# Optimization experiments

Hardware: AMD Instinct MI355X
Metric: run time of the kernel (lower is better)

Reference implementation:

```python
import jax, jax.numpy as jnp
import numpy as np

B, S, D, H = 2, 2048, 1024, 16  # batch, pad_size, depth, num_heads
HD = D // H


def setup_inputs() -> dict:
    key = jax.random.key(0)
    ks = jax.random.split(key, 20)
    g = lambda k, shape, fan: jax.random.normal(k, shape, jnp.float32) * np.sqrt(2.0 / fan)
    return {
        "x": jax.random.normal(ks[0], (B, S, D), jnp.float32),
        "W_in": g(ks[1], (D, D), 2 * D), "b_in": g(ks[2], (D,), D),
        "Wq": g(ks[3], (D, D), 2 * D), "bq": g(ks[4], (D,), D),
        "Wk": g(ks[5], (D, D), 2 * D), "bk": g(ks[6], (D,), D),
        "Wv": g(ks[7], (D, D), 2 * D), "bv": g(ks[8], (D,), D),
        "Wo": g(ks[9], (D, D), 2 * D), "bo": g(ks[10], (D,), D),
        "W1": g(ks[11], (D, D), 2 * D), "b1": g(ks[12], (D,), D),
        "W2": g(ks[13], (D, D), 2 * D), "b2": g(ks[14], (D,), D),
        # residual gate scalars (random_id_att / random_id_ff); zero-init in the
        # original, set nonzero here so the whole graph contributes.
        "s_att": jax.random.normal(ks[15], (), jnp.float32),
        "s_ff": jax.random.normal(ks[16], (), jnp.float32),
    }


def reference(x, W_in, b_in, Wq, bq, Wk, bk, Wv, bv, Wo, bo, W1, b1, W2, b2, s_att, s_ff):
    # input projection
    h = x @ W_in + b_in                                   # [B,S,D]
    # QKV projections, split heads -> [B,H,S,HD]
    def heads(t):
        return t.reshape(B, S, H, HD).transpose(0, 2, 1, 3)
    q = heads(h @ Wq + bq)
    k = heads(h @ Wk + bk)
    v = heads(h @ Wv + bv)
    # attention: sigmoid(logits) * tanh(logits) instead of softmax
    logits = jnp.einsum("bhqd,bhkd->bhqk", q, k) / jnp.sqrt(jnp.float32(D))
    attn = jax.nn.sigmoid(logits) * jnp.tanh(logits)      # [B,H,S,S]
    ctx = jnp.einsum("bhqk,bhkd->bhqd", attn, v)
    ctx = ctx.transpose(0, 2, 1, 3).reshape(B, S, D)
    attention = ctx @ Wo + bo
    # gated residual 1
    latent = h + s_att * attention
    # FFN (depth -> depth -> depth), leaky_relu alpha=0.2 (tf default);
    # dropout treated as identity (inference)
    ff = jax.nn.leaky_relu(latent @ W1 + b1, negative_slope=0.2) @ W2 + b2
    out = latent + s_ff * ff
    return out
```

## Files before the change

kernel.cpp:

```cpp
#include <hip/hip_runtime.h>
#include <cstdint>
#include <cstddef>


#define B_ 2
#define S_ 2048
#define D_ 1024
#define H_ 16
#define M_ 4096

typedef __attribute__((ext_vector_type(4))) float  f32x4;
typedef __attribute__((ext_vector_type(8))) __bf16 bf16x8;
typedef __attribute__((ext_vector_type(4))) __bf16 bf16x4;

__device__ __forceinline__ void async16(const void* g, void* l) {
    __builtin_amdgcn_global_load_lds(
        (__attribute__((address_space(1))) void*)(g),
        (__attribute__((address_space(3))) void*)(l), 16, 0, 0);
}

__device__ __forceinline__ float actf(float s) {
    float t = fminf(s * -0.045084223f, 21.6f);
    float u = __builtin_amdgcn_exp2f(t);
    return (1.f - u) * __builtin_amdgcn_rcpf(1.f + u * u);
}

template <int BM, int EPI>
__global__ __launch_bounds__(256) void gemm_k(
    const __bf16* __restrict__ A, const __bf16* __restrict__ Bt,
    const float* __restrict__ bias, const __bf16* __restrict__ aux,
    const float* __restrict__ scal, void* __restrict__ out, int Ntot)
{
    constexpr int K = D_;
    constexpr int MF = BM / 32;
    __shared__ __align__(16) __bf16 As[2][BM][64];
    __shared__ __align__(16) __bf16 Bs[2][128][64];

    const int tid = threadIdx.x, wid = tid >> 6, lane = tid & 63;
    const int wr = wid >> 1, wc = wid & 1;
    const int m0 = blockIdx.x * BM, n0 = blockIdx.y * 128;
    const int frow = lane & 15;
    const int kb = (lane >> 4) * 16;
    char* cAs = (char*)As; char* cBs = (char*)Bs;

    f32x4 acc[MF][4] = {};

    auto stage = [&](int buf, int k0) {
        char* lA = cAs + buf * (BM * 128);
        char* lB = cBs + buf * (128 * 128);
#pragma unroll
        for (int i = 0; i < MF; ++i) {
            const int o = tid * 16 + i * 4096;
            const int row = o >> 7;
            const int cb = (o & 127) ^ ((row & 7) << 4);
            async16(A + (size_t)(m0 + row) * K + k0 + (cb >> 1), lA + o);
        }
#pragma unroll
        for (int i = 0; i < 4; ++i) {
            const int o = tid * 16 + i * 4096;
            const int row = o >> 7;
            const int cb = (o & 127) ^ ((row & 7) << 4);
            async16(Bt + (size_t)(n0 + row) * K + k0 + (cb >> 1), lB + o);
        }
    };

    stage(0, 0);
    __syncthreads();
    int cur = 0;

    for (int k0 = 0; k0 < K; k0 += 64) {
        if (k0 + 64 < K) stage(cur ^ 1, k0 + 64);
        char* lA = cAs + cur * (BM * 128);
        char* lB = cBs + cur * (128 * 128);
#pragma unroll
        for (int kk = 0; kk < 2; ++kk) {
            bf16x8 af[MF], bfr[4];
#pragma unroll
            for (int m = 0; m < MF; ++m) {
                const int r = wr * (BM / 2) + m * 16 + frow;
                af[m] = *(const bf16x8*)(lA + ((r * 128 + kk * 64 + kb) ^ ((r & 7) << 4)));
            }
#pragma unroll
            for (int n = 0; n < 4; ++n) {
                const int r = wc * 64 + n * 16 + frow;
                bfr[n] = *(const bf16x8*)(lB + ((r * 128 + kk * 64 + kb) ^ ((r & 7) << 4)));
            }
#pragma unroll
            for (int m = 0; m < MF; ++m)
#pragma unroll
                for (int n = 0; n < 4; ++n)
                    acc[m][n] = __builtin_amdgcn_mfma_f32_16x16x32_bf16(
                        af[m], bfr[n], acc[m][n], 0, 0, 0);
        }
        __syncthreads();
        cur ^= 1;
    }

    const float sv = (EPI >= 2) ? *scal : 0.f;
#pragma unroll
    for (int m = 0; m < MF; ++m) {
#pragma unroll
        for (int n = 0; n < 4; ++n) {
#pragma unroll
            for (int r = 0; r < 4; ++r) {
                const int row = m0 + wr * (BM / 2) + m * 16 + (lane >> 4) * 4 + r;
                const int col = n0 + wc * 64 + n * 16 + frow;
                const size_t idx = (size_t)row * Ntot + col;
                float v = acc[m][n][r] + bias[col];
                if constexpr (EPI == 0) {
                    ((__bf16*)out)[idx] = (__bf16)v;
                } else if constexpr (EPI == 1) {
                    v = v > 0.f ? v : 0.2f * v;
                    ((__bf16*)out)[idx] = (__bf16)v;
                } else if constexpr (EPI == 2) {
                    ((__bf16*)out)[idx] = (__bf16)((float)aux[idx] + sv * v);
                } else {
                    ((float*)out)[idx] = (float)aux[idx] + sv * v;
                }
            }
        }
    }
}

__global__ __launch_bounds__(256, 4) void attn_k(
    const __bf16* __restrict__ Q, const __bf16* __restrict__ Kmat,
    const __bf16* __restrict__ VT, __bf16* __restrict__ CTX, int ld)
{
    __shared__ __align__(16) __bf16 Ks[2][64][64];
    __shared__ __align__(16) __bf16 Vs[2][64][64];
    __shared__ __align__(16) __bf16 Ps[64][64];

    const int tid = threadIdx.x, wid = tid >> 6, lane = tid & 63;
    const int qt = blockIdx.x, h = blockIdx.y, b = blockIdx.z;
    const int q0 = qt * 64;
    const int frow = lane & 15, g = lane >> 4;
    const int kg8 = g * 8, kb = g * 16;
    const int qrow = wid * 16 + frow;

    const __bf16* qbase = Q    + (size_t)(b * S_ + q0) * ld + h * 64;
    const __bf16* kbase = Kmat + (size_t)b * S_ * ld + h * 64;
    const __bf16* vbase = VT   + (size_t)(b * H_ + h) * 64 * S_;

    bf16x8 qf[2];
#pragma unroll
    for (int kk = 0; kk < 2; ++kk)
        qf[kk] = *(const bf16x8*)(qbase + (size_t)qrow * ld + kk * 32 + kg8);

    f32x4 octx[4] = {};
    char* cKs = (char*)Ks; char* cVs = (char*)Vs; char* lPs = (char*)Ps;

    auto stageKV = [&](int buf, int kt) {
#pragma unroll
        for (int i = 0; i < 2; ++i) {
            const int o = tid * 16 + i * 4096;
            const int row = o >> 7;
            const int cb = (o & 127) ^ ((row & 7) << 4);
            async16(kbase + (size_t)(kt + row) * ld + (cb >> 1),
                    cKs + buf * 8192 + o);
            async16(vbase + (size_t)row * S_ + kt + (cb >> 1),
                    cVs + buf * 8192 + o);
        }
    };

    stageKV(0, 0);
    __syncthreads();
    int cur = 0;

    for (int kt = 0; kt < S_; kt += 64) {
        if (kt + 64 < S_) stageKV(cur ^ 1, kt + 64);
        char* lKs = cKs + cur * 8192;
        char* lVs = cVs + cur * 8192;

        f32x4 scc[4] = {};
#pragma unroll
        for (int kk = 0; kk < 2; ++kk) {
            bf16x8 kf[4];
#pragma unroll
            for (int n = 0; n < 4; ++n) {
                const int r = n * 16 + frow;
                kf[n] = *(const bf16x8*)(lKs + ((r * 128 + kk * 64 + kb) ^ ((r & 7) << 4)));
            }
#pragma unroll
            for (int n = 0; n < 4; ++n)
                scc[n] = __builtin_amdgcn_mfma_f32_16x16x32_bf16(
                    kf[n], qf[kk], scc[n], 0, 0, 0);
        }

#pragma unroll
        for (int n = 0; n < 4; ++n) {
            bf16x4 pw;
#pragma unroll
            for (int r = 0; r < 4; ++r) pw[r] = (__bf16)actf(scc[n][r]);
            *(bf16x4*)(lPs + ((qrow * 128 + n * 32 + g * 8) ^ ((qrow & 7) << 4))) = pw;
        }

#pragma unroll
        for (int ks = 0; ks < 2; ++ks) {
            bf16x8 pf = *(const bf16x8*)(lPs +
                ((qrow * 128 + ks * 64 + kb) ^ ((qrow & 7) << 4)));
            bf16x8 vf[4];
#pragma unroll
            for (int nd = 0; nd < 4; ++nd) {
                const int rd = nd * 16 + frow;
                vf[nd] = *(const bf16x8*)(lVs + ((rd * 128 + ks * 64 + kb) ^ ((rd & 7) << 4)));
            }
#pragma unroll
            for (int nd = 0; nd < 4; ++nd)
                octx[nd] = __builtin_amdgcn_mfma_f32_16x16x32_bf16(
                    pf, vf[nd], octx[nd], 0, 0, 0);
        }
        __syncthreads();
        cur ^= 1;
    }

#pragma unroll
    for (int nd = 0; nd < 4; ++nd)
#pragma unroll
        for (int r = 0; r < 4; ++r) {
            const int row = q0 + wid * 16 + g * 4 + r;
            const int col = h * 64 + nd * 16 + frow;
            CTX[(size_t)(b * S_ + row) * D_ + col] = (__bf16)octx[nd][r];
        }
}

struct WPack { const float* w[7]; };

__global__ __launch_bounds__(256) void conv_transpose_w(WPack p, __bf16* out) {
    __shared__ float t[32][33];
    const float* W = p.w[blockIdx.z];
    __bf16* o = out + (size_t)blockIdx.z * D_ * D_;
    const int c0 = blockIdx.x * 32, r0 = blockIdx.y * 32;
    const int tx = threadIdx.x, ty = threadIdx.y;
#pragma unroll
    for (int i = 0; i < 4; ++i)
        t[ty + i * 8][tx] = W[(size_t)(r0 + ty + i * 8) * D_ + c0 + tx];
    __syncthreads();
#pragma unroll
    for (int i = 0; i < 4; ++i)
        o[(size_t)(c0 + ty + i * 8) * D_ + r0 + tx] = (__bf16)t[tx][ty + i * 8];
}

__global__ __launch_bounds__(256) void conv_bf16(
    const float* __restrict__ in, __bf16* __restrict__ out, int n4)
{
    const int i = blockIdx.x * blockDim.x + threadIdx.x;
    if (i < n4) {
        f32x4 v = ((const f32x4*)in)[i];
        bf16x4 o;
        o[0] = (__bf16)v[0]; o[1] = (__bf16)v[1];
        o[2] = (__bf16)v[2]; o[3] = (__bf16)v[3];
        ((bf16x4*)out)[i] = o;
    }
}

__global__ __launch_bounds__(256) void bcat_k(
    const float* __restrict__ bq, const float* __restrict__ bk,
    const float* __restrict__ bv, float* __restrict__ o)
{
    const int i = blockIdx.x * 256 + threadIdx.x;
    o[i] = i < 1024 ? bq[i] : (i < 2048 ? bk[i - 1024] : bv[i - 2048]);
}

__global__ __launch_bounds__(256) void transpose_v(
    const __bf16* __restrict__ V, __bf16* __restrict__ VT, int ld)
{
    __shared__ __bf16 t[32][33];
    const int s0 = blockIdx.x * 32, c0 = blockIdx.y * 32, b = blockIdx.z;
    const int tx = threadIdx.x, ty = threadIdx.y;
#pragma unroll
    for (int i = 0; i < 4; ++i)
        t[ty + i * 8][tx] = V[(size_t)(b * S_ + s0 + ty + i * 8) * ld + c0 + tx];
    __syncthreads();
#pragma unroll
    for (int i = 0; i < 4; ++i)
        VT[(size_t)(b * D_ + c0 + ty + i * 8) * S_ + s0 + tx] = t[tx][ty + i * 8];
}

extern "C" void kernel_launch(void* const* d_in, const int* in_sizes, int n_in,
                              void* d_out, int out_size, void* d_ws, size_t ws_size,
                              hipStream_t stream) {
    const float* x    = (const float*)d_in[0];
    const float* W_in = (const float*)d_in[1];
    const float* b_in = (const float*)d_in[2];
    const float* Wq   = (const float*)d_in[3];
    const float* bq   = (const float*)d_in[4];
    const float* Wk   = (const float*)d_in[5];
    const float* bk   = (const float*)d_in[6];
    const float* Wv   = (const float*)d_in[7];
    const float* bv   = (const float*)d_in[8];
    const float* Wo   = (const float*)d_in[9];
    const float* bo   = (const float*)d_in[10];
    const float* W1   = (const float*)d_in[11];
    const float* b1   = (const float*)d_in[12];
    const float* W2   = (const float*)d_in[13];
    const float* b2   = (const float*)d_in[14];
    const float* s_att = (const float*)d_in[15];
    const float* s_ff  = (const float*)d_in[16];

    char* ws = (char*)d_ws;
    const size_t WB = (size_t)D_ * D_ * 2;
    const size_t MB = (size_t)M_ * D_ * 2;
    __bf16* WT   = (__bf16*)(ws);
    __bf16* Hb   = (__bf16*)(ws + 7 * WB);
    __bf16* QKVb = (__bf16*)(ws + 7 * WB + MB);
    __bf16* VTb  = (__bf16*)(ws + 7 * WB + 4 * MB);
    __bf16* Xb   = (__bf16*)(ws + 7 * WB + 5 * MB);
    float*  bcat = (float*)VTb;
    __bf16* CTXb = Xb;
    __bf16* LATb = QKVb;
    __bf16* FF1b = QKVb + (size_t)M_ * D_;
    auto WTi = [&](int i) { return WT + (size_t)i * D_ * D_; };

    WPack wp;
    wp.w[0] = W_in; wp.w[1] = Wq; wp.w[2] = Wk; wp.w[3] = Wv;
    wp.w[4] = Wo;   wp.w[5] = W1; wp.w[6] = W2;
    conv_transpose_w<<<dim3(32, 32, 7), dim3(32, 8), 0, stream>>>(wp, WT);
    conv_bf16<<<dim3(4096), dim3(256), 0, stream>>>(x, Xb, (M_ * D_) / 4);
    bcat_k<<<dim3(12), dim3(256), 0, stream>>>(bq, bk, bv, bcat);

    gemm_k<64, 0><<<dim3(64, 8), dim3(256), 0, stream>>>(
        Xb, WTi(0), b_in, nullptr, nullptr, Hb, D_);
    gemm_k<128, 0><<<dim3(32, 24), dim3(256), 0, stream>>>(
        Hb, WTi(1), bcat, nullptr, nullptr, QKVb, 3 * D_);
    transpose_v<<<dim3(64, 32, 2), dim3(32, 8), 0, stream>>>(
        QKVb + 2 * D_, VTb, 3 * D_);
    attn_k<<<dim3(32, 16, 2), dim3(256), 0, stream>>>(
        QKVb, QKVb + D_, VTb, CTXb, 3 * D_);
    gemm_k<64, 2><<<dim3(64, 8), dim3(256), 0, stream>>>(
        CTXb, WTi(4), bo, Hb, s_att, LATb, D_);
    gemm_k<64, 1><<<dim3(64, 8), dim3(256), 0, stream>>>(
        LATb, WTi(5), b1, nullptr, nullptr, FF1b, D_);
    gemm_k<64, 3><<<dim3(64, 8), dim3(256), 0, stream>>>(
        FF1b, WTi(6), b2, LATb, s_ff, d_out, D_);
}
```

Before: 299.0 us.

## Use fine-grained vmcnt pipelining, XCD-aware block remap, and 128x128 GEMM tiles

```diff
diff --git a/kernel.cpp b/kernel.cpp
--- a/kernel.cpp
+++ b/kernel.cpp
@@ -13,6 +13,8 @@
 typedef __attribute__((ext_vector_type(8))) __bf16 bf16x8;
 typedef __attribute__((ext_vector_type(4))) __bf16 bf16x4;
 
+#define WAITVM(N) asm volatile("s_waitcnt vmcnt(" #N ")" ::: "memory")
+
 __device__ __forceinline__ void async16(const void* g, void* l) {
     __builtin_amdgcn_global_load_lds(
         (__attribute__((address_space(1))) void*)(g),
@@ -25,59 +27,51 @@
     return (1.f - u) * __builtin_amdgcn_rcpf(1.f + u * u);
 }
 
-template <int BM, int EPI>
+template <int EPI>
 __global__ __launch_bounds__(256) void gemm_k(
     const __bf16* __restrict__ A, const __bf16* __restrict__ Bt,
     const float* __restrict__ bias, const __bf16* __restrict__ aux,
     const float* __restrict__ scal, void* __restrict__ out, int Ntot)
 {
     constexpr int K = D_;
-    constexpr int MF = BM / 32;
-    __shared__ __align__(16) __bf16 As[2][BM][64];
+    __shared__ __align__(16) __bf16 As[2][128][64];
     __shared__ __align__(16) __bf16 Bs[2][128][64];
 
-    const int tid = threadIdx.x, wid = tid >> 6, lane = tid & 63;
+    const int tid = threadIdx.x, lane = tid & 63, wid = tid >> 6;
     const int wr = wid >> 1, wc = wid & 1;
-    const int m0 = blockIdx.x * BM, n0 = blockIdx.y * 128;
+    const int cpx = (int)gridDim.x >> 3;
+    const int bid = (int)blockIdx.x;
+    const int wg = (bid & 7) * cpx + (bid >> 3);
+    const int m0 = (wg & 31) * 128;
+    const int n0 = (wg >> 5) * 128;
     const int frow = lane & 15;
     const int kb = (lane >> 4) * 16;
     char* cAs = (char*)As; char* cBs = (char*)Bs;
 
-    f32x4 acc[MF][4] = {};
+    f32x4 acc[4][4] = {};
 
     auto stage = [&](int buf, int k0) {
-        char* lA = cAs + buf * (BM * 128);
-        char* lB = cBs + buf * (128 * 128);
-#pragma unroll
-        for (int i = 0; i < MF; ++i) {
-            const int o = tid * 16 + i * 4096;
-            const int row = o >> 7;
-            const int cb = (o & 127) ^ ((row & 7) << 4);
-            async16(A + (size_t)(m0 + row) * K + k0 + (cb >> 1), lA + o);
-        }
 #pragma unroll
         for (int i = 0; i < 4; ++i) {
             const int o = tid * 16 + i * 4096;
             const int row = o >> 7;
             const int cb = (o & 127) ^ ((row & 7) << 4);
-            async16(Bt + (size_t)(n0 + row) * K + k0 + (cb >> 1), lB + o);
+            async16(A + (size_t)(m0 + row) * K + k0 + (cb >> 1),
+                    cAs + buf * 16384 + o);
+            async16(Bt + (size_t)(n0 + row) * K + k0 + (cb >> 1),
+                    cBs + buf * 16384 + o);
         }
     };
 
-    stage(0, 0);
-    __syncthreads();
-    int cur = 0;
-
-    for (int k0 = 0; k0 < K; k0 += 64) {
-        if (k0 + 64 < K) stage(cur ^ 1, k0 + 64);
-        char* lA = cAs + cur * (BM * 128);
-        char* lB = cBs + cur * (128 * 128);
+    auto compute = [&](int buf) {
+        char* lA = cAs + buf * 16384;
+        char* lB = cBs + buf * 16384;
 #pragma unroll
         for (int kk = 0; kk < 2; ++kk) {
-            bf16x8 af[MF], bfr[4];
-#pragma unroll
-            for (int m = 0; m < MF; ++m) {
-                const int r = wr * (BM / 2) + m * 16 + frow;
+            bf16x8 af[4], bfr[4];
+#pragma unroll
+            for (int m = 0; m < 4; ++m) {
+                const int r = wr * 64 + m * 16 + frow;
                 af[m] = *(const bf16x8*)(lA + ((r * 128 + kk * 64 + kb) ^ ((r & 7) << 4)));
             }
 #pragma unroll
@@ -86,24 +80,43 @@
                 bfr[n] = *(const bf16x8*)(lB + ((r * 128 + kk * 64 + kb) ^ ((r & 7) << 4)));
             }
 #pragma unroll
-            for (int m = 0; m < MF; ++m)
+            for (int m = 0; m < 4; ++m)
 #pragma unroll
                 for (int n = 0; n < 4; ++n)
                     acc[m][n] = __builtin_amdgcn_mfma_f32_16x16x32_bf16(
                         af[m], bfr[n], acc[m][n], 0, 0, 0);
         }
-        __syncthreads();
-        cur ^= 1;
+    };
+
+    stage(0, 0);
+    stage(1, 64);
+    WAITVM(8);
+    __builtin_amdgcn_sched_barrier(0);
+    __builtin_amdgcn_s_barrier();
+
+    for (int tp = 0; tp < 8; ++tp) {
+        const int t0 = tp * 2;
+        compute(0);
+        __builtin_amdgcn_s_barrier();
+        if (t0 < 14) { stage(0, (t0 + 2) * 64); WAITVM(8); }
+        else         { WAITVM(0); }
+        __builtin_amdgcn_sched_barrier(0);
+        __builtin_amdgcn_s_barrier();
+        compute(1);
+        __builtin_amdgcn_s_barrier();
+        if (t0 < 14) { stage(1, (t0 + 3) * 64); WAITVM(8); }
+        __builtin_amdgcn_sched_barrier(0);
+        __builtin_amdgcn_s_barrier();
     }
 
     const float sv = (EPI >= 2) ? *scal : 0.f;
 #pragma unroll
-    for (int m = 0; m < MF; ++m) {
+    for (int m = 0; m < 4; ++m) {
 #pragma unroll
         for (int n = 0; n < 4; ++n) {
 #pragma unroll
             for (int r = 0; r < 4; ++r) {
-                const int row = m0 + wr * (BM / 2) + m * 16 + (lane >> 4) * 4 + r;
+                const int row = m0 + wr * 64 + m * 16 + (lane >> 4) * 4 + r;
                 const int col = n0 + wc * 64 + n * 16 + frow;
                 const size_t idx = (size_t)row * Ntot + col;
                 float v = acc[m][n][r] + bias[col];
@@ -131,7 +144,9 @@
     __shared__ __align__(16) __bf16 Ps[64][64];
 
     const int tid = threadIdx.x, wid = tid >> 6, lane = tid & 63;
-    const int qt = blockIdx.x, h = blockIdx.y, b = blockIdx.z;
+    const int bid = (int)blockIdx.x;
+    const int wg = (bid & 7) * 128 + (bid >> 3);
+    const int qt = wg & 31, h = (wg >> 5) & 15, b = wg >> 9;
     const int q0 = qt * 64;
     const int frow = lane & 15, g = lane >> 4;
     const int kg8 = g * 8, kb = g * 16;
@@ -145,6 +160,7 @@
 #pragma unroll
     for (int kk = 0; kk < 2; ++kk)
         qf[kk] = *(const bf16x8*)(qbase + (size_t)qrow * ld + kk * 32 + kg8);
+    __builtin_amdgcn_sched_barrier(0);
 
     f32x4 octx[4] = {};
     char* cKs = (char*)Ks; char* cVs = (char*)Vs; char* lPs = (char*)Ps;
@@ -162,16 +178,9 @@
         }
     };
 
-    stageKV(0, 0);
-    __syncthreads();
-    int cur = 0;
-
-    for (int kt = 0; kt < S_; kt += 64) {
-        if (kt + 64 < S_) stageKV(cur ^ 1, kt + 64);
-        char* lKs = cKs + cur * 8192;
-        char* lVs = cVs + cur * 8192;
-
+    auto computeTile = [&](char* lKs, char* lVs) {
         f32x4 scc[4] = {};
+        __builtin_amdgcn_s_setprio(1);
 #pragma unroll
         for (int kk = 0; kk < 2; ++kk) {
             bf16x8 kf[4];
@@ -185,7 +194,7 @@
                 scc[n] = __builtin_amdgcn_mfma_f32_16x16x32_bf16(
                     kf[n], qf[kk], scc[n], 0, 0, 0);
         }
-
+        __builtin_amdgcn_s_setprio(0);
 #pragma unroll
         for (int n = 0; n < 4; ++n) {
             bf16x4 pw;
@@ -193,7 +202,7 @@
             for (int r = 0; r < 4; ++r) pw[r] = (__bf16)actf(scc[n][r]);
             *(bf16x4*)(lPs + ((qrow * 128 + n * 32 + g * 8) ^ ((qrow & 7) << 4))) = pw;
         }
-
+        __builtin_amdgcn_s_setprio(1);
 #pragma unroll
         for (int ks = 0; ks < 2; ++ks) {
             bf16x8 pf = *(const bf16x8*)(lPs +
@@ -209,8 +218,28 @@
                 octx[nd] = __builtin_amdgcn_mfma_f32_16x16x32_bf16(
                     pf, vf[nd], octx[nd], 0, 0, 0);
         }
-        __syncthreads();
-        cur ^= 1;
+        __builtin_amdgcn_s_setprio(0);
+    };
+
+    stageKV(0, 0);
+    stageKV(1, 64);
+    WAITVM(4);
+    __builtin_amdgcn_sched_barrier(0);
+    __builtin_amdgcn_s_barrier();
+
+    for (int it = 0; it < 16; ++it) {
+        const int kt0 = it * 128;
+        computeTile(cKs, cVs);
+        __builtin_amdgcn_s_barrier();
+        if (it < 15) { stageKV(0, kt0 + 128); WAITVM(4); }
+        else         { WAITVM(0); }
+        __builtin_amdgcn_sched_barrier(0);
+        __builtin_amdgcn_s_barrier();
+        computeTile(cKs + 8192, cVs + 8192);
+        __builtin_amdgcn_s_barrier();
+        if (it < 15) { stageKV(1, kt0 + 192); WAITVM(4); }
+        __builtin_amdgcn_sched_barrier(0);
+        __builtin_amdgcn_s_barrier();
     }
 
 #pragma unroll
@@ -318,18 +347,18 @@
     conv_bf16<<<dim3(4096), dim3(256), 0, stream>>>(x, Xb, (M_ * D_) / 4);
     bcat_k<<<dim3(12), dim3(256), 0, stream>>>(bq, bk, bv, bcat);
 
-    gemm_k<64, 0><<<dim3(64, 8), dim3(256), 0, stream>>>(
+    gemm_k<0><<<dim3(256), dim3(256), 0, stream>>>(
         Xb, WTi(0), b_in, nullptr, nullptr, Hb, D_);
-    gemm_k<128, 0><<<dim3(32, 24), dim3(256), 0, stream>>>(
+    gemm_k<0><<<dim3(768), dim3(256), 0, stream>>>(
         Hb, WTi(1), bcat, nullptr, nullptr, QKVb, 3 * D_);
     transpose_v<<<dim3(64, 32, 2), dim3(32, 8), 0, stream>>>(
         QKVb + 2 * D_, VTb, 3 * D_);
-    attn_k<<<dim3(32, 16, 2), dim3(256), 0, stream>>>(
+    attn_k<<<dim3(1024), dim3(256), 0, stream>>>(
         QKVb, QKVb + D_, VTb, CTXb, 3 * D_);
-    gemm_k<64, 2><<<dim3(64, 8), dim3(256), 0, stream>>>(
+    gemm_k<2><<<dim3(256), dim3(256), 0, stream>>>(
         CTXb, WTi(4), bo, Hb, s_att, LATb, D_);
-    gemm_k<64, 1><<<dim3(64, 8), dim3(256), 0, stream>>>(
+    gemm_k<1><<<dim3(256), dim3(256), 0, stream>>>(
         LATb, WTi(5), b1, nullptr, nullptr, FF1b, D_);
-    gemm_k<64, 3><<<dim3(64, 8), dim3(256), 0, stream>>>(
+    gemm_k<3><<<dim3(256), dim3(256), 0, stream>>>(
         FF1b, WTi(6), b2, LATb, s_ff, d_out, D_);
 }
```

Measured after the change: 290.7 us. 2.8% less time.
